# Kernel tuning notes

Measured on AMD Instinct MI355X. Metric: run time of the kernel, lower is better.

Reference implementation:

```python
import jax, jax.numpy as jnp
import numpy as np

N_EMBD = 384
N_HEAD = 6
HEAD_SIZE = N_EMBD // N_HEAD  # 64
B, T, S = 128, 256, 256
EPS = 1e-5


def setup_inputs() -> dict:
    key = jax.random.key(0)
    ks = jax.random.split(key, 20)
    w = lambda k, shape: (jax.random.normal(k, shape, dtype=jnp.float32) * 0.02)
    inp = {
        'x': jax.random.normal(ks[0], (B, T, N_EMBD), dtype=jnp.float32),
        'encoder_output': jax.random.normal(ks[1], (B, S, N_EMBD), dtype=jnp.float32),
        # masked self-attention heads (stacked over heads): [H, C, D]
        'wq1': w(ks[2], (N_HEAD, N_EMBD, HEAD_SIZE)),
        'wk1': w(ks[3], (N_HEAD, N_EMBD, HEAD_SIZE)),
        'wv1': w(ks[4], (N_HEAD, N_EMBD, HEAD_SIZE)),
        'proj1_w': w(ks[5], (N_EMBD, N_EMBD)),
        'proj1_b': jnp.zeros((N_EMBD,), jnp.float32),
        # cross-attention heads
        'wq2': w(ks[6], (N_HEAD, N_EMBD, HEAD_SIZE)),
        'wk2': w(ks[7], (N_HEAD, N_EMBD, HEAD_SIZE)),
        'wv2': w(ks[8], (N_HEAD, N_EMBD, HEAD_SIZE)),
        'proj2_w': w(ks[9], (N_EMBD, N_EMBD)),
        'proj2_b': jnp.zeros((N_EMBD,), jnp.float32),
        # feed-forward
        'ffn_w1': w(ks[10], (N_EMBD, 4 * N_EMBD)),
        'ffn_b1': jnp.zeros((4 * N_EMBD,), jnp.float32),
        'ffn_w2': w(ks[11], (4 * N_EMBD, N_EMBD)),
        'ffn_b2': jnp.zeros((N_EMBD,), jnp.float32),
        # layernorms
        'ln1_g': jnp.ones((N_EMBD,), jnp.float32), 'ln1_b': jnp.zeros((N_EMBD,), jnp.float32),
        'ln2_g': jnp.ones((N_EMBD,), jnp.float32), 'ln2_b': jnp.zeros((N_EMBD,), jnp.float32),
        'ln3_g': jnp.ones((N_EMBD,), jnp.float32), 'ln3_b': jnp.zeros((N_EMBD,), jnp.float32),
    }
    return inp


def _layernorm(x, g, b):
    mu = jnp.mean(x, axis=-1, keepdims=True)
    var = jnp.mean(jnp.square(x - mu), axis=-1, keepdims=True)
    return (x - mu) * jax.lax.rsqrt(var + EPS) * g + b


def _mha(xq, xkv, wq, wk, wv, proj_w, proj_b, causal):
    # NOTE: source scales by C**-0.5 with C = n_embd (not head_size)
    scale = jnp.asarray(N_EMBD, xq.dtype) ** -0.5
    q = jnp.einsum('btc,hcd->bhtd', xq, wq)
    k = jnp.einsum('bsc,hcd->bhsd', xkv, wk)
    v = jnp.einsum('bsc,hcd->bhsd', xkv, wv)
    wei = jnp.einsum('bhtd,bhsd->bhts', q, k) * scale
    if causal:
        Tq, Tk = xq.shape[1], xkv.shape[1]
        mask = jnp.tril(jnp.ones((Tq, Tk), dtype=bool))
        wei = jnp.where(mask, wei, jnp.asarray(-jnp.inf, wei.dtype))
    p = jax.nn.softmax(wei, axis=-1)  # dropout omitted (eval mode)
    o = jnp.einsum('bhts,bhsd->bhtd', p, v)
    Bq, H, Tq, D = o.shape
    o = o.transpose(0, 2, 1, 3).reshape(Bq, Tq, H * D)  # concat heads
    return o @ proj_w + proj_b


def reference(x, encoder_output,
              wq1, wk1, wv1, proj1_w, proj1_b,
              wq2, wk2, wv2, proj2_w, proj2_b,
              ffn_w1, ffn_b1, ffn_w2, ffn_b2,
              ln1_g, ln1_b, ln2_g, ln2_b, ln3_g, ln3_b):
    # x = x + masked self-attn(ln1(x))
    x = x + _mha(_layernorm(x, ln1_g, ln1_b), _layernorm(x, ln1_g, ln1_b),
                 wq1, wk1, wv1, proj1_w, proj1_b, causal=True)
    # x = x + cross-attn(ln2(x), encoder_output)  (no mask)
    x = x + _mha(_layernorm(x, ln2_g, ln2_b), encoder_output,
                 wq2, wk2, wv2, proj2_w, proj2_b, causal=False)
    # x = x + ffwd(ln3(x))
    h = _layernorm(x, ln3_g, ln3_b)
    x = x + (jax.nn.relu(h @ ffn_w1 + ffn_b1) @ ffn_w2 + ffn_b2)
    return x
```

## Files before the change

kernel.cpp:

```cpp
#include <hip/hip_runtime.h>
#include <hip/hip_bf16.h>

#define BB 128
#define TT 256
#define CC 384
#define HH 6
#define DD 64
#define NTOK 32768

typedef __attribute__((ext_vector_type(8))) short short8;
typedef __attribute__((ext_vector_type(4))) float f32x4;

__device__ __forceinline__ unsigned short f2bf(float f) {
  union { float f; unsigned int u; } v; v.f = f;
  unsigned int r = v.u + 0x7fff + ((v.u >> 16) & 1);
  return (unsigned short)(r >> 16);
}

__device__ __forceinline__ void glds16(const void* g, void* l) {
  __builtin_amdgcn_global_load_lds((const __attribute__((address_space(1))) void*)g,
                                   (__attribute__((address_space(3))) void*)l, 16, 0, 0);
}

__device__ __forceinline__ void vm_drain() {
  asm volatile("s_waitcnt vmcnt(0)" ::: "memory");
  __builtin_amdgcn_sched_barrier(0);
}

__global__ __launch_bounds__(256) void pack_t_k(
    const float* __restrict__ wq1, const float* __restrict__ wk1, const float* __restrict__ wv1,
    const float* __restrict__ wq2, const float* __restrict__ wk2, const float* __restrict__ wv2,
    const float* __restrict__ proj1_w, const float* __restrict__ proj2_w,
    const float* __restrict__ ffn_w1, const float* __restrict__ ffn_w2,
    unsigned short* __restrict__ W) {
  __shared__ unsigned short tile[64 * 72];
  const int id = blockIdx.x;
  const int tid = threadIdx.x;
  const float* src;
  unsigned short* dst;
  int ldIn, ldOut, i0, j0;
  if (id < 216) {
    int w = id / 36, rem = id - w * 36;
    int h = rem / 6, tr = rem - h * 6;
    const float* bases[6] = {wq1, wk1, wv1, wq2, wk2, wv2};
    const int dstOff[6] = {0, 147456, 294912, 442368, 589824, 737280};
    src = bases[w] + h * 24576;
    dst = W + dstOff[w] + h * 24576;
    ldIn = 64; ldOut = 384; i0 = tr * 64; j0 = 0;
  } else if (id < 288) {
    int t = id - 216;
    int which = t / 36; t -= which * 36;
    int tr = t / 6, tc = t - tr * 6;
    src = which ? proj2_w : proj1_w;
    dst = W + (which ? 1032192 : 884736);
    ldIn = 384; ldOut = 384; i0 = tr * 64; j0 = tc * 64;
  } else if (id < 432) {
    int t = id - 288;
    int tr = t / 24, tc = t - tr * 24;
    src = ffn_w1; dst = W + 1179648;
    ldIn = 1536; ldOut = 384; i0 = tr * 64; j0 = tc * 64;
  } else {
    int t = id - 432;
    int tr = t / 6, tc = t - tr * 6;
    src = ffn_w2; dst = W + 1769472;
    ldIn = 384; ldOut = 1536; i0 = tr * 64; j0 = tc * 64;
  }
#pragma unroll
  for (int p = 0; p < 4; ++p) {
    int chunk = p * 256 + tid;
    int r = chunk >> 4, c4 = chunk & 15;
    float4 f = *(const float4*)&src[(size_t)(i0 + r) * ldIn + j0 + c4 * 4];
    tile[(c4 * 4 + 0) * 72 + r] = f2bf(f.x);
    tile[(c4 * 4 + 1) * 72 + r] = f2bf(f.y);
    tile[(c4 * 4 + 2) * 72 + r] = f2bf(f.z);
    tile[(c4 * 4 + 3) * 72 + r] = f2bf(f.w);
  }
  __syncthreads();
#pragma unroll
  for (int p = 0; p < 2; ++p) {
    int chunk = p * 256 + tid;
    int j = chunk >> 3, i8 = chunk & 7;
    *(uint4*)&dst[(size_t)(j0 + j) * ldOut + i0 + i8 * 8] = *(const uint4*)&tile[j * 72 + i8 * 8];
  }
}

__global__ __launch_bounds__(256) void ln_k(const float* __restrict__ x,
                                            unsigned short* __restrict__ out,
                                            const float* __restrict__ gamma,
                                            const float* __restrict__ beta) {
  int row = blockIdx.x * 4 + (threadIdx.x >> 6);
  int lane = threadIdx.x & 63;
  const float* xr = x + (size_t)row * CC;
  float v[6];
  float s = 0.f;
#pragma unroll
  for (int j = 0; j < 6; ++j) { v[j] = xr[j * 64 + lane]; s += v[j]; }
#pragma unroll
  for (int m = 1; m < 64; m <<= 1) s += __shfl_xor(s, m);
  float mu = s * (1.0f / CC);
  float vs = 0.f;
#pragma unroll
  for (int j = 0; j < 6; ++j) { float d = v[j] - mu; vs += d * d; }
#pragma unroll
  for (int m = 1; m < 64; m <<= 1) vs += __shfl_xor(vs, m);
  float rs = rsqrtf(vs * (1.0f / CC) + 1e-5f);
  unsigned short* orow = out + (size_t)row * CC;
#pragma unroll
  for (int j = 0; j < 6; ++j) {
    int cidx = j * 64 + lane;
    orow[cidx] = f2bf((v[j] - mu) * rs * gamma[cidx] + beta[cidx]);
  }
}

template <int EPI, bool AF32, int BM>
__global__ __launch_bounds__(256) void gemm_k(const void* __restrict__ Ap, int lda,
                                              const unsigned short* __restrict__ Bt, int ldb,
                                              void* __restrict__ Cp, int ldc,
                                              const float* __restrict__ bias,
                                              const float* __restrict__ res, int ldres,
                                              int K, int nx) {
  constexpr int MI = BM / 32;
  constexpr int APASS = BM * 8 / 256;
  constexpr int SMEMN = (EPI == 2) ? (BM * 256) : (BM * 64 + 8192);
  __shared__ unsigned short smem[SMEMN];
  unsigned short* sA = smem;
  unsigned short* sB = smem + BM * 64;
  const int tid = threadIdx.x;
  const int chunkg = gridDim.x >> 3;
  const int wg = blockIdx.x;
  const int lg = (wg & 7) * chunkg + (wg >> 3);
  const int bx = lg % nx, by = lg / nx;
  const int m0 = by * BM;
  const int n0 = bx * 128;
  const int wid = tid >> 6, lane = tid & 63;
  const int wr = wid >> 1, wc = wid & 1;
  const int g = lane >> 4, c = lane & 15;

  f32x4 acc[MI][4] = {};
  float biasr[4];
  if (EPI >= 1) {
#pragma unroll
    for (int ni = 0; ni < 4; ++ni) biasr[ni] = bias[n0 + wc * 64 + ni * 16 + c];
  }

  const int nt = K >> 6;
  for (int t = 0; t < nt; ++t) {
    const int k0 = t * 64;
    if constexpr (!AF32) {
#pragma unroll
      for (int p = 0; p < APASS; ++p) {
        int chunk = p * 256 + tid;
        int row = chunk >> 3, grp = chunk & 7;
        const unsigned short* Ab = (const unsigned short*)Ap;
        glds16(&Ab[(size_t)(m0 + row) * lda + k0 + ((grp ^ (row & 7)) << 3)], &sA[chunk * 8]);
      }
    } else {
#pragma unroll
      for (int p = 0; p < APASS; ++p) {
        int chunk = p * 256 + tid;
        int row = chunk >> 3, grp = chunk & 7;
        int dst = row * 64 + ((grp ^ (row & 7)) << 3);
        const float* Af = (const float*)Ap + (size_t)(m0 + row) * lda + k0 + grp * 8;
        float4 f0 = *(const float4*)Af;
        float4 f1 = *(const float4*)(Af + 4);
        union { unsigned short h[8]; uint4 u; } t2;
        t2.h[0] = f2bf(f0.x); t2.h[1] = f2bf(f0.y); t2.h[2] = f2bf(f0.z); t2.h[3] = f2bf(f0.w);
        t2.h[4] = f2bf(f1.x); t2.h[5] = f2bf(f1.y); t2.h[6] = f2bf(f1.z); t2.h[7] = f2bf(f1.w);
        *(uint4*)&sA[dst] = t2.u;
      }
    }
#pragma unroll
    for (int p = 0; p < 4; ++p) {
      int chunk = p * 256 + tid;
      int row = chunk >> 3, grp = chunk & 7;
      glds16(&Bt[(size_t)(n0 + row) * ldb + k0 + ((grp ^ (row & 7)) << 3)], &sB[chunk * 8]);
    }
    vm_drain();
    __syncthreads();
#pragma unroll
    for (int kk = 0; kk < 2; ++kk) {
      short8 a[MI], b[4];
#pragma unroll
      for (int mi = 0; mi < MI; ++mi) {
        int r = wr * (BM / 2) + mi * 16 + c;
        a[mi] = *(const short8*)&sA[r * 64 + (((kk * 4 + g) ^ (r & 7)) << 3)];
      }
#pragma unroll
      for (int ni = 0; ni < 4; ++ni) {
        int rb = wc * 64 + ni * 16 + c;
        b[ni] = *(const short8*)&sB[rb * 64 + (((kk * 4 + g) ^ (rb & 7)) << 3)];
      }
#pragma unroll
      for (int mi = 0; mi < MI; ++mi)
#pragma unroll
        for (int ni = 0; ni < 4; ++ni)
          acc[mi][ni] = __builtin_amdgcn_mfma_f32_16x16x32_bf16(a[mi], b[ni], acc[mi][ni], 0, 0, 0);
    }
    __syncthreads();
  }

  if (EPI <= 1) {
#pragma unroll
    for (int mi = 0; mi < MI; ++mi)
#pragma unroll
      for (int ni = 0; ni < 4; ++ni)
#pragma unroll
        for (int i = 0; i < 4; ++i) {
          int row = wr * (BM / 2) + mi * 16 + g * 4 + i;
          int col = wc * 64 + ni * 16 + c;
          float v = acc[mi][ni][i];
          if (EPI == 1) v = fmaxf(v + biasr[ni], 0.f);
          int gsw = (col >> 3) ^ ((row >> 2) & 7);
          smem[row * 128 + gsw * 8 + (col & 7)] = f2bf(v);
        }
    __syncthreads();
#pragma unroll
    for (int it = 0; it < BM / 16; ++it) {
      int chunk = it * 256 + tid;
      int row = chunk >> 4, c16 = chunk & 15;
      int gsw = c16 ^ ((row >> 2) & 7);
      *(uint4*)&((unsigned short*)Cp)[(size_t)(m0 + row) * ldc + n0 + c16 * 8] =
          *(const uint4*)&smem[row * 128 + gsw * 8];
    }
  } else {
    float* smf = (float*)smem;
#pragma unroll
    for (int mi = 0; mi < MI; ++mi)
#pragma unroll
      for (int ni = 0; ni < 4; ++ni)
#pragma unroll
        for (int i = 0; i < 4; ++i) {
          int row = wr * (BM / 2) + mi * 16 + g * 4 + i;
          int col = wc * 64 + ni * 16 + c;
          int gg = col >> 2;
          int sg = gg ^ (row & 7);
          smf[row * 128 + sg * 4 + (col & 3)] = acc[mi][ni][i] + biasr[ni];
        }
    __syncthreads();
#pragma unroll
    for (int it = 0; it < BM / 8; ++it) {
      int chunk = it * 256 + tid;
      int row = chunk >> 5, gg = chunk & 31;
      int sg = gg ^ (row & 7);
      float4 v = *(const float4*)&smf[row * 128 + sg * 4];
      float4 r = *(const float4*)&res[(size_t)(m0 + row) * ldres + n0 + gg * 4];
      float4 o;
      o.x = v.x + r.x; o.y = v.y + r.y; o.z = v.z + r.z; o.w = v.w + r.w;
      *(float4*)&((float*)Cp)[(size_t)(m0 + row) * ldc + n0 + gg * 4] = o;
    }
  }
}

__device__ __forceinline__ int vt_off(int d, int sgrp) {
  return d * 256 + ((((sgrp + (d >> 3)) & 31) ^ (d & 7)) << 3);
}

template <bool CAUSAL>
__global__ __launch_bounds__(512, 2) void attn_k(const unsigned short* __restrict__ QKV,
                                                 unsigned short* __restrict__ O) {
  __shared__ unsigned short Ks[256 * 64];
  __shared__ unsigned short Vt[64 * 256];
  __shared__ unsigned short Ps[8][16 * 40];
  const int bh = blockIdx.x >> 1;
  const int half = blockIdx.x & 1;
  const int b = bh / HH, hh = bh - b * HH;
  const int tid = threadIdx.x, wid = tid >> 6, lane = tid & 63;
  const int g = lane >> 4, c = lane & 15;
  const unsigned short* base = QKV + (size_t)b * TT * 1152;

#pragma unroll
  for (int t = 0; t < 4; ++t) {
    int chunk = t * 512 + tid;
    int s = chunk >> 3, grp = chunk & 7;
    *(uint4*)&Ks[s * 64 + ((grp ^ (s & 7)) << 3)] =
        *(const uint4*)&base[(size_t)s * 1152 + 384 + hh * 64 + grp * 8];
    union { unsigned short h[8]; uint4 u; } tv;
    tv.u = *(const uint4*)&base[(size_t)s * 1152 + 768 + hh * 64 + grp * 8];
#pragma unroll
    for (int j = 0; j < 8; ++j) Vt[vt_off(grp * 8 + j, s >> 3) + (s & 7)] = tv.h[j];
  }
  __syncthreads();

  const float scale = 0.05103103630798287f;
  unsigned short* Pw = &Ps[wid][0];
  const int qr0 = half * 128 + wid * 16;

  short8 aq[2];
#pragma unroll
  for (int kk = 0; kk < 2; ++kk)
    aq[kk] = *(const short8*)&QKV[(size_t)(b * TT + qr0 + c) * 1152 + hh * 64 + kk * 32 + g * 8];

  f32x4 sacc[16] = {};
#pragma unroll
  for (int sj = 0; sj < 16; ++sj) {
    if (!CAUSAL || sj * 16 <= qr0) {
      int rk = sj * 16 + c;
      f32x4 z = sacc[sj];
      z = __builtin_amdgcn_mfma_f32_16x16x32_bf16(
          aq[0], *(const short8*)&Ks[rk * 64 + ((g ^ (rk & 7)) << 3)], z, 0, 0, 0);
      z = __builtin_amdgcn_mfma_f32_16x16x32_bf16(
          aq[1], *(const short8*)&Ks[rk * 64 + (((4 + g) ^ (rk & 7)) << 3)], z, 0, 0, 0);
      sacc[sj] = z;
    }
  }

  float inv[4];
#pragma unroll
  for (int i = 0; i < 4; ++i) {
    const int qr = qr0 + g * 4 + i;
    float mx = -1e30f;
#pragma unroll
    for (int sj = 0; sj < 16; ++sj) {
      if (!CAUSAL || sj * 16 <= qr0) {
        int s = sj * 16 + c;
        float v = sacc[sj][i] * scale;
        if (CAUSAL && s > qr) v = -1e30f;
        sacc[sj][i] = v;
        mx = fmaxf(mx, v);
      }
    }
#pragma unroll
    for (int m = 1; m < 16; m <<= 1) mx = fmaxf(mx, __shfl_xor(mx, m));
    float sum = 0.f;
#pragma unroll
    for (int sj = 0; sj < 16; ++sj) {
      if (!CAUSAL || sj * 16 <= qr0) {
        float p = __expf(sacc[sj][i] - mx);
        sacc[sj][i] = p;
        sum += p;
      }
    }
#pragma unroll
    for (int m = 1; m < 16; m <<= 1) sum += __shfl_xor(sum, m);
    inv[i] = 1.0f / sum;
  }

  f32x4 oacc[4] = {};
#pragma unroll
  for (int sk = 0; sk < 8; ++sk) {
    if (!CAUSAL || sk * 32 <= qr0) {
#pragma unroll
      for (int half_sj = 0; half_sj < 2; ++half_sj) {
        int sj = sk * 2 + half_sj;
#pragma unroll
        for (int i = 0; i < 4; ++i)
          Pw[(g * 4 + i) * 40 + half_sj * 16 + c] = f2bf(sacc[sj][i]);
      }
      short8 ap = *(const short8*)&Pw[c * 40 + g * 8];
#pragma unroll
      for (int dj = 0; dj < 4; ++dj) {
        short8 bv = *(const short8*)&Vt[vt_off(dj * 16 + c, sk * 4 + g)];
        oacc[dj] = __builtin_amdgcn_mfma_f32_16x16x32_bf16(ap, bv, oacc[dj], 0, 0, 0);
      }
    }
  }

  __syncthreads();
#pragma unroll
  for (int dj = 0; dj < 4; ++dj)
#pragma unroll
    for (int i = 0; i < 4; ++i) {
      int lr = wid * 16 + g * 4 + i;
      int col = dj * 16 + c;
      int gsw = (col >> 3) ^ ((lr >> 2) & 7);
      Ks[lr * 64 + gsw * 8 + (col & 7)] = f2bf(oacc[dj][i] * inv[i]);
    }
  __syncthreads();
#pragma unroll
  for (int it = 0; it < 2; ++it) {
    int chunk = it * 512 + tid;
    int row = chunk >> 3, c8 = chunk & 7;
    int gsw = c8 ^ ((row >> 2) & 7);
    *(uint4*)&O[(size_t)(b * TT + half * 128 + row) * CC + hh * 64 + c8 * 8] =
        *(const uint4*)&Ks[row * 64 + gsw * 8];
  }
}

extern "C" void kernel_launch(void* const* d_in, const int* in_sizes, int n_in,
                              void* d_out, int out_size, void* d_ws, size_t ws_size,
                              hipStream_t stream) {
  const float* x = (const float*)d_in[0];
  const float* enc = (const float*)d_in[1];
  const float* wq1 = (const float*)d_in[2];
  const float* wk1 = (const float*)d_in[3];
  const float* wv1 = (const float*)d_in[4];
  const float* proj1_w = (const float*)d_in[5];
  const float* proj1_b = (const float*)d_in[6];
  const float* wq2 = (const float*)d_in[7];
  const float* wk2 = (const float*)d_in[8];
  const float* wv2 = (const float*)d_in[9];
  const float* proj2_w = (const float*)d_in[10];
  const float* proj2_b = (const float*)d_in[11];
  const float* ffn_w1 = (const float*)d_in[12];
  const float* ffn_b1 = (const float*)d_in[13];
  const float* ffn_w2 = (const float*)d_in[14];
  const float* ffn_b2 = (const float*)d_in[15];
  const float* ln1_g = (const float*)d_in[16];
  const float* ln1_b = (const float*)d_in[17];
  const float* ln2_g = (const float*)d_in[18];
  const float* ln2_b = (const float*)d_in[19];
  const float* ln3_g = (const float*)d_in[20];
  const float* ln3_b = (const float*)d_in[21];
  float* out = (float*)d_out;

  char* ws = (char*)d_ws;
  const size_t OFF_A = 0;
  const size_t OFF_X = 50331648;
  const size_t OFF_Q = 75497472;
  const size_t OFF_O = 150994944;
  const size_t OFF_W = 176160768;

  float* xc = (float*)(ws + OFF_A);
  unsigned short* xn = (unsigned short*)(ws + OFF_X);
  unsigned short* qkv = (unsigned short*)(ws + OFF_Q);
  unsigned short* h1 = (unsigned short*)(ws + OFF_Q);
  unsigned short* obuf = (unsigned short*)(ws + OFF_O);
  unsigned short* W = (unsigned short*)(ws + OFF_W);

  unsigned short* Wqkv1t = W + 0;
  unsigned short* Wq2t = W + 442368;
  unsigned short* Wkv2t = W + 589824;
  unsigned short* proj1t = W + 884736;
  unsigned short* proj2t = W + 1032192;
  unsigned short* W1t = W + 1179648;
  unsigned short* W2t = W + 1769472;

  pack_t_k<<<576, 256, 0, stream>>>(wq1, wk1, wv1, wq2, wk2, wv2,
                                    proj1_w, proj2_w, ffn_w1, ffn_w2, W);

  dim3 blk(256);
  ln_k<<<8192, blk, 0, stream>>>(x, xn, ln1_g, ln1_b);
  gemm_k<0, false, 128><<<2304, blk, 0, stream>>>(xn, 384, Wqkv1t, 384, qkv, 1152,
                                                  nullptr, nullptr, 0, 384, 9);
  attn_k<true><<<1536, 512, 0, stream>>>(qkv, obuf);
  gemm_k<2, false, 64><<<1536, blk, 0, stream>>>(obuf, 384, proj1t, 384, xc, 384,
                                                 proj1_b, x, 384, 384, 3);
  ln_k<<<8192, blk, 0, stream>>>(xc, xn, ln2_g, ln2_b);
  gemm_k<0, false, 128><<<768, blk, 0, stream>>>(xn, 384, Wq2t, 384, qkv, 1152,
                                                 nullptr, nullptr, 0, 384, 3);
  gemm_k<0, true, 128><<<1536, blk, 0, stream>>>(enc, 384, Wkv2t, 384, qkv + 384, 1152,
                                                 nullptr, nullptr, 0, 384, 6);
  attn_k<false><<<1536, 512, 0, stream>>>(qkv, obuf);
  gemm_k<2, false, 64><<<1536, blk, 0, stream>>>(obuf, 384, proj2t, 384, xc, 384,
                                                 proj2_b, xc, 384, 384, 3);
  ln_k<<<8192, blk, 0, stream>>>(xc, xn, ln3_g, ln3_b);
  gemm_k<1, false, 128><<<3072, blk, 0, stream>>>(xn, 384, W1t, 384, h1, 1536,
                                                  ffn_b1, nullptr, 0, 384, 12);
  gemm_k<2, false, 64><<<1536, blk, 0, stream>>>(h1, 1536, W2t, 1536, out, 384,
                                                 ffn_b2, xc, 384, 1536, 3);
}
```

Measured before the change: 399.7 us.

## Double-buffer GEMM LDS tiles, shrink BM to 64, vectorize layernorm

The bf16-input GEMM path now double-buffers A/B tiles in LDS, issuing the next tile's global-to-LDS loads before computing the current one and waiting with a partial vmcnt. This hides global load latency that the old drain-then-compute loop exposed. Several GEMM launches switch from BM=128 to BM=64 with twice the blocks, trading per-block reuse for more parallelism and lower LDS/register use. The layernorm kernel also moves to float2 loads and packed 32-bit bf16 stores.

```diff
diff --git a/kernel.cpp b/kernel.cpp
--- a/kernel.cpp
+++ b/kernel.cpp
@@ -90,25 +90,32 @@
                                             const float* __restrict__ beta) {
   int row = blockIdx.x * 4 + (threadIdx.x >> 6);
   int lane = threadIdx.x & 63;
-  const float* xr = x + (size_t)row * CC;
-  float v[6];
+  const float2* xr = (const float2*)(x + (size_t)row * CC);
+  float2 v[3];
   float s = 0.f;
 #pragma unroll
-  for (int j = 0; j < 6; ++j) { v[j] = xr[j * 64 + lane]; s += v[j]; }
+  for (int j = 0; j < 3; ++j) { v[j] = xr[j * 64 + lane]; s += v[j].x + v[j].y; }
 #pragma unroll
   for (int m = 1; m < 64; m <<= 1) s += __shfl_xor(s, m);
   float mu = s * (1.0f / CC);
   float vs = 0.f;
 #pragma unroll
-  for (int j = 0; j < 6; ++j) { float d = v[j] - mu; vs += d * d; }
+  for (int j = 0; j < 3; ++j) {
+    float dx = v[j].x - mu, dy = v[j].y - mu;
+    vs += dx * dx + dy * dy;
+  }
 #pragma unroll
   for (int m = 1; m < 64; m <<= 1) vs += __shfl_xor(vs, m);
   float rs = rsqrtf(vs * (1.0f / CC) + 1e-5f);
-  unsigned short* orow = out + (size_t)row * CC;
-#pragma unroll
-  for (int j = 0; j < 6; ++j) {
+  unsigned int* orow = (unsigned int*)(out + (size_t)row * CC);
+#pragma unroll
+  for (int j = 0; j < 3; ++j) {
     int cidx = j * 64 + lane;
-    orow[cidx] = f2bf((v[j] - mu) * rs * gamma[cidx] + beta[cidx]);
+    float2 gmm = ((const float2*)gamma)[cidx];
+    float2 bt = ((const float2*)beta)[cidx];
+    unsigned int lo = f2bf((v[j].x - mu) * rs * gmm.x + bt.x);
+    unsigned int hi = f2bf((v[j].y - mu) * rs * gmm.y + bt.y);
+    orow[cidx] = lo | (hi << 16);
   }
 }
 
@@ -121,10 +128,9 @@
                                               int K, int nx) {
   constexpr int MI = BM / 32;
   constexpr int APASS = BM * 8 / 256;
-  constexpr int SMEMN = (EPI == 2) ? (BM * 256) : (BM * 64 + 8192);
+  constexpr int LOADS = APASS + 4;
+  constexpr int SMEMN = AF32 ? (BM * 64 + 8192) : 2 * (BM * 64 + 8192);
   __shared__ unsigned short smem[SMEMN];
-  unsigned short* sA = smem;
-  unsigned short* sB = smem + BM * 64;
   const int tid = threadIdx.x;
   const int chunkg = gridDim.x >> 3;
   const int wg = blockIdx.x;
@@ -142,19 +148,85 @@
 #pragma unroll
     for (int ni = 0; ni < 4; ++ni) biasr[ni] = bias[n0 + wc * 64 + ni * 16 + c];
   }
-
   const int nt = K >> 6;
-  for (int t = 0; t < nt; ++t) {
+
+  auto stageAB = [&](int t, unsigned short* sAb, unsigned short* sBb) {
     const int k0 = t * 64;
-    if constexpr (!AF32) {
-#pragma unroll
-      for (int p = 0; p < APASS; ++p) {
-        int chunk = p * 256 + tid;
-        int row = chunk >> 3, grp = chunk & 7;
-        const unsigned short* Ab = (const unsigned short*)Ap;
-        glds16(&Ab[(size_t)(m0 + row) * lda + k0 + ((grp ^ (row & 7)) << 3)], &sA[chunk * 8]);
-      }
-    } else {
+#pragma unroll
+    for (int p = 0; p < APASS; ++p) {
+      int chunk = p * 256 + tid;
+      int row = chunk >> 3, grp = chunk & 7;
+      const unsigned short* Ab = (const unsigned short*)Ap;
+      glds16(&Ab[(size_t)(m0 + row) * lda + k0 + ((grp ^ (row & 7)) << 3)], &sAb[chunk * 8]);
+    }
+#pragma unroll
+    for (int p = 0; p < 4; ++p) {
+      int chunk = p * 256 + tid;
+      int row = chunk >> 3, grp = chunk & 7;
+      glds16(&Bt[(size_t)(n0 + row) * ldb + k0 + ((grp ^ (row & 7)) << 3)], &sBb[chunk * 8]);
+    }
+  };
+  auto computeT = [&](const unsigned short* sAb, const unsigned short* sBb) {
+#pragma unroll
+    for (int kk = 0; kk < 2; ++kk) {
+      short8 a[MI], b[4];
+#pragma unroll
+      for (int mi = 0; mi < MI; ++mi) {
+        int r = wr * (BM / 2) + mi * 16 + c;
+        a[mi] = *(const short8*)&sAb[r * 64 + (((kk * 4 + g) ^ (r & 7)) << 3)];
+      }
+#pragma unroll
+      for (int ni = 0; ni < 4; ++ni) {
+        int rb = wc * 64 + ni * 16 + c;
+        b[ni] = *(const short8*)&sBb[rb * 64 + (((kk * 4 + g) ^ (rb & 7)) << 3)];
+      }
+#pragma unroll
+      for (int mi = 0; mi < MI; ++mi)
+#pragma unroll
+        for (int ni = 0; ni < 4; ++ni)
+          acc[mi][ni] = __builtin_amdgcn_mfma_f32_16x16x32_bf16(a[mi], b[ni], acc[mi][ni], 0, 0, 0);
+    }
+  };
+
+  if constexpr (!AF32) {
+    unsigned short* sA0 = smem;
+    unsigned short* sB0 = smem + BM * 64;
+    unsigned short* sA1 = smem + BM * 64 + 8192;
+    unsigned short* sB1 = sA1 + BM * 64;
+    stageAB(0, sA0, sB0);
+    int t = 0;
+    for (;;) {
+      if (t + 1 < nt) {
+        stageAB(t + 1, sA1, sB1);
+        asm volatile("s_waitcnt vmcnt(%0)" ::"i"(LOADS) : "memory");
+      } else {
+        asm volatile("s_waitcnt vmcnt(0)" ::: "memory");
+      }
+      __builtin_amdgcn_sched_barrier(0);
+      __builtin_amdgcn_s_barrier();
+      computeT(sA0, sB0);
+      if (t + 1 >= nt) break;
+      __builtin_amdgcn_s_barrier();
+      ++t;
+      if (t + 1 < nt) {
+        stageAB(t + 1, sA0, sB0);
+        asm volatile("s_waitcnt vmcnt(%0)" ::"i"(LOADS) : "memory");
+      } else {
+        asm volatile("s_waitcnt vmcnt(0)" ::: "memory");
+      }
+      __builtin_amdgcn_sched_barrier(0);
+      __builtin_amdgcn_s_barrier();
+      computeT(sA1, sB1);
+      if (t + 1 >= nt) break;
+      __builtin_amdgcn_s_barrier();
+      ++t;
+    }
+    __builtin_amdgcn_s_barrier();
+  } else {
+    unsigned short* sA = smem;
+    unsigned short* sB = smem + BM * 64;
+    for (int t = 0; t < nt; ++t) {
+      const int k0 = t * 64;
 #pragma unroll
       for (int p = 0; p < APASS; ++p) {
         int chunk = p * 256 + tid;
@@ -168,35 +240,17 @@
         t2.h[4] = f2bf(f1.x); t2.h[5] = f2bf(f1.y); t2.h[6] = f2bf(f1.z); t2.h[7] = f2bf(f1.w);
         *(uint4*)&sA[dst] = t2.u;
       }
-    }
-#pragma unroll
-    for (int p = 0; p < 4; ++p) {
-      int chunk = p * 256 + tid;
-      int row = chunk >> 3, grp = chunk & 7;
-      glds16(&Bt[(size_t)(n0 + row) * ldb + k0 + ((grp ^ (row & 7)) << 3)], &sB[chunk * 8]);
-    }
-    vm_drain();
-    __syncthreads();
-#pragma unroll
-    for (int kk = 0; kk < 2; ++kk) {
-      short8 a[MI], b[4];
-#pragma unroll
-      for (int mi = 0; mi < MI; ++mi) {
-        int r = wr * (BM / 2) + mi * 16 + c;
-        a[mi] = *(const short8*)&sA[r * 64 + (((kk * 4 + g) ^ (r & 7)) << 3)];
-      }
-#pragma unroll
-      for (int ni = 0; ni < 4; ++ni) {
-        int rb = wc * 64 + ni * 16 + c;
-        b[ni] = *(const short8*)&sB[rb * 64 + (((kk * 4 + g) ^ (rb & 7)) << 3)];
-      }
-#pragma unroll
-      for (int mi = 0; mi < MI; ++mi)
-#pragma unroll
-        for (int ni = 0; ni < 4; ++ni)
-          acc[mi][ni] = __builtin_amdgcn_mfma_f32_16x16x32_bf16(a[mi], b[ni], acc[mi][ni], 0, 0, 0);
-    }
-    __syncthreads();
+#pragma unroll
+      for (int p = 0; p < 4; ++p) {
+        int chunk = p * 256 + tid;
+        int row = chunk >> 3, grp = chunk & 7;
+        glds16(&Bt[(size_t)(n0 + row) * ldb + k0 + ((grp ^ (row & 7)) << 3)], &sB[chunk * 8]);
+      }
+      vm_drain();
+      __syncthreads();
+      computeT(sA, sB);
+      __syncthreads();
+    }
   }
 
   if (EPI <= 1) {
@@ -430,13 +484,13 @@
 
   dim3 blk(256);
   ln_k<<<8192, blk, 0, stream>>>(x, xn, ln1_g, ln1_b);
-  gemm_k<0, false, 128><<<2304, blk, 0, stream>>>(xn, 384, Wqkv1t, 384, qkv, 1152,
-                                                  nullptr, nullptr, 0, 384, 9);
+  gemm_k<0, false, 64><<<4608, blk, 0, stream>>>(xn, 384, Wqkv1t, 384, qkv, 1152,
+                                                 nullptr, nullptr, 0, 384, 9);
   attn_k<true><<<1536, 512, 0, stream>>>(qkv, obuf);
   gemm_k<2, false, 64><<<1536, blk, 0, stream>>>(obuf, 384, proj1t, 384, xc, 384,
                                                  proj1_b, x, 384, 384, 3);
   ln_k<<<8192, blk, 0, stream>>>(xc, xn, ln2_g, ln2_b);
-  gemm_k<0, false, 128><<<768, blk, 0, stream>>>(xn, 384, Wq2t, 384, qkv, 1152,
+  gemm_k<0, false, 64><<<1536, blk, 0, stream>>>(xn, 384, Wq2t, 384, qkv, 1152,
                                                  nullptr, nullptr, 0, 384, 3);
   gemm_k<0, true, 128><<<1536, blk, 0, stream>>>(enc, 384, Wkv2t, 384, qkv + 384, 1152,
                                                  nullptr, nullptr, 0, 384, 6);
@@ -444,8 +498,8 @@
   gemm_k<2, false, 64><<<1536, blk, 0, stream>>>(obuf, 384, proj2t, 384, xc, 384,
                                                  proj2_b, xc, 384, 384, 3);
   ln_k<<<8192, blk, 0, stream>>>(xc, xn, ln3_g, ln3_b);
-  gemm_k<1, false, 128><<<3072, blk, 0, stream>>>(xn, 384, W1t, 384, h1, 1536,
-                                                  ffn_b1, nullptr, 0, 384, 12);
+  gemm_k<1, false, 64><<<6144, blk, 0, stream>>>(xn, 384, W1t, 384, h1, 1536,
+                                                 ffn_b1, nullptr, 0, 384, 12);
   gemm_k<2, false, 64><<<1536, blk, 0, stream>>>(h1, 1536, W2t, 1536, out, 384,
                                                  ffn_b2, xc, 384, 1536, 3);
 }
```

After: 410.8 us. +2.8%, slower.

## Fuse projection GEMM with residual add and following LayerNorm

Applied to the files above, without the earlier changes.

Adds a gemm_ln_k kernel in which each block computes a full 64x384 output row tile of the attention projection, adds bias and residual, writes the fp32 residual stream, and computes the next LayerNorm in the epilogue using a cross-wave partial sum reduction before writing bf16 normalized output. This removes two separate LayerNorm launches and their reread of the residual stream. The fused kernel runs only 512 blocks with a single-buffered K loop, so occupancy and latency hiding may be worse than the old GEMM. The variance is computed as E[x^2]-mu^2, which is less numerically robust. The remaining ln_k is also vectorized to float2 loads and packed bf16 stores.

```diff
diff --git a/kernel.cpp b/kernel.cpp
--- a/kernel.cpp
+++ b/kernel.cpp
@@ -90,25 +90,32 @@
                                             const float* __restrict__ beta) {
   int row = blockIdx.x * 4 + (threadIdx.x >> 6);
   int lane = threadIdx.x & 63;
-  const float* xr = x + (size_t)row * CC;
-  float v[6];
+  const float2* xr = (const float2*)(x + (size_t)row * CC);
+  float2 v[3];
   float s = 0.f;
 #pragma unroll
-  for (int j = 0; j < 6; ++j) { v[j] = xr[j * 64 + lane]; s += v[j]; }
+  for (int j = 0; j < 3; ++j) { v[j] = xr[j * 64 + lane]; s += v[j].x + v[j].y; }
 #pragma unroll
   for (int m = 1; m < 64; m <<= 1) s += __shfl_xor(s, m);
   float mu = s * (1.0f / CC);
   float vs = 0.f;
 #pragma unroll
-  for (int j = 0; j < 6; ++j) { float d = v[j] - mu; vs += d * d; }
+  for (int j = 0; j < 3; ++j) {
+    float dx = v[j].x - mu, dy = v[j].y - mu;
+    vs += dx * dx + dy * dy;
+  }
 #pragma unroll
   for (int m = 1; m < 64; m <<= 1) vs += __shfl_xor(vs, m);
   float rs = rsqrtf(vs * (1.0f / CC) + 1e-5f);
-  unsigned short* orow = out + (size_t)row * CC;
-#pragma unroll
-  for (int j = 0; j < 6; ++j) {
+  unsigned int* orow = (unsigned int*)(out + (size_t)row * CC);
+#pragma unroll
+  for (int j = 0; j < 3; ++j) {
     int cidx = j * 64 + lane;
-    orow[cidx] = f2bf((v[j] - mu) * rs * gamma[cidx] + beta[cidx]);
+    float2 gmm = ((const float2*)gamma)[cidx];
+    float2 bt = ((const float2*)beta)[cidx];
+    unsigned int lo = f2bf((v[j].x - mu) * rs * gmm.x + bt.x);
+    unsigned int hi = f2bf((v[j].y - mu) * rs * gmm.y + bt.y);
+    orow[cidx] = lo | (hi << 16);
   }
 }
 
@@ -248,6 +255,153 @@
       o.x = v.x + r.x; o.y = v.y + r.y; o.z = v.z + r.z; o.w = v.w + r.w;
       *(float4*)&((float*)Cp)[(size_t)(m0 + row) * ldc + n0 + gg * 4] = o;
     }
+  }
+}
+
+__global__ __launch_bounds__(512, 2) void gemm_ln_k(
+    const unsigned short* __restrict__ Ab, const unsigned short* __restrict__ Bt,
+    const float* __restrict__ bias, const float* __restrict__ res,
+    float* __restrict__ xc, const float* __restrict__ gamma,
+    const float* __restrict__ beta, unsigned short* __restrict__ xn) {
+  __shared__ unsigned short smem[28672];
+  __shared__ float part[64][8];
+  unsigned short* sA = smem;
+  unsigned short* sB = smem + 4096;
+  const int tid = threadIdx.x;
+  const int chunkg = gridDim.x >> 3;
+  const int wg = blockIdx.x;
+  const int lg = (wg & 7) * chunkg + (wg >> 3);
+  const int m0 = lg * 64;
+  const int wid = tid >> 6, lane = tid & 63;
+  const int wr = wid >> 2, wcg = wid & 3;
+  const int g = lane >> 4, c = lane & 15;
+
+  f32x4 acc[2][6] = {};
+  float biasr[6], gam[6], bet[6];
+#pragma unroll
+  for (int ni = 0; ni < 6; ++ni) {
+    int col = wcg * 96 + ni * 16 + c;
+    biasr[ni] = bias[col]; gam[ni] = gamma[col]; bet[ni] = beta[col];
+  }
+
+  for (int t = 0; t < 6; ++t) {
+    const int k0 = t * 64;
+    {
+      int chunk = tid;
+      int row = chunk >> 3, grp = chunk & 7;
+      glds16(&Ab[(size_t)(m0 + row) * 384 + k0 + ((grp ^ (row & 7)) << 3)], &sA[chunk * 8]);
+    }
+#pragma unroll
+    for (int p = 0; p < 6; ++p) {
+      int chunk = p * 512 + tid;
+      int row = chunk >> 3, grp = chunk & 7;
+      glds16(&Bt[(size_t)row * 384 + k0 + ((grp ^ (row & 7)) << 3)], &sB[chunk * 8]);
+    }
+    vm_drain();
+    __syncthreads();
+#pragma unroll
+    for (int kk = 0; kk < 2; ++kk) {
+      short8 a[2], b[6];
+#pragma unroll
+      for (int mi = 0; mi < 2; ++mi) {
+        int r = wr * 32 + mi * 16 + c;
+        a[mi] = *(const short8*)&sA[r * 64 + (((kk * 4 + g) ^ (r & 7)) << 3)];
+      }
+#pragma unroll
+      for (int ni = 0; ni < 6; ++ni) {
+        int rb = wcg * 96 + ni * 16 + c;
+        b[ni] = *(const short8*)&sB[rb * 64 + (((kk * 4 + g) ^ (rb & 7)) << 3)];
+      }
+#pragma unroll
+      for (int mi = 0; mi < 2; ++mi)
+#pragma unroll
+        for (int ni = 0; ni < 6; ++ni)
+          acc[mi][ni] = __builtin_amdgcn_mfma_f32_16x16x32_bf16(a[mi], b[ni], acc[mi][ni], 0, 0, 0);
+    }
+    __syncthreads();
+  }
+
+#pragma unroll
+  for (int mi = 0; mi < 2; ++mi)
+#pragma unroll
+    for (int i = 0; i < 4; ++i) {
+      int row = m0 + wr * 32 + mi * 16 + g * 4 + i;
+#pragma unroll
+      for (int ni = 0; ni < 6; ++ni)
+        acc[mi][ni][i] += biasr[ni] + res[(size_t)row * 384 + wcg * 96 + ni * 16 + c];
+    }
+
+#pragma unroll
+  for (int mi = 0; mi < 2; ++mi)
+#pragma unroll
+    for (int i = 0; i < 4; ++i) {
+      float s = 0.f, q = 0.f;
+#pragma unroll
+      for (int ni = 0; ni < 6; ++ni) { float v = acc[mi][ni][i]; s += v; q += v * v; }
+#pragma unroll
+      for (int m = 1; m < 16; m <<= 1) { s += __shfl_xor(s, m); q += __shfl_xor(q, m); }
+      if (c == 0) {
+        int lr = wr * 32 + mi * 16 + g * 4 + i;
+        part[lr][wcg] = s;
+        part[lr][4 + wcg] = q;
+      }
+    }
+  __syncthreads();
+  float mu[2][4], rs[2][4];
+#pragma unroll
+  for (int mi = 0; mi < 2; ++mi)
+#pragma unroll
+    for (int i = 0; i < 4; ++i) {
+      int lr = wr * 32 + mi * 16 + g * 4 + i;
+      float s = part[lr][0] + part[lr][1] + part[lr][2] + part[lr][3];
+      float q = part[lr][4] + part[lr][5] + part[lr][6] + part[lr][7];
+      float m_ = s * (1.0f / 384.f);
+      mu[mi][i] = m_;
+      rs[mi][i] = rsqrtf(q * (1.0f / 384.f) - m_ * m_ + 1e-5f);
+    }
+
+  float* bf = (float*)smem;
+#pragma unroll
+  for (int h = 0; h < 2; ++h) {
+    __syncthreads();
+    if (wr == h) {
+#pragma unroll
+      for (int mi = 0; mi < 2; ++mi)
+#pragma unroll
+        for (int ni = 0; ni < 6; ++ni)
+#pragma unroll
+          for (int i = 0; i < 4; ++i) {
+            int lr = mi * 16 + g * 4 + i;
+            bf[lr * 388 + wcg * 96 + ni * 16 + c] = acc[mi][ni][i];
+          }
+    }
+    __syncthreads();
+#pragma unroll
+    for (int p = 0; p < 6; ++p) {
+      int chunk = p * 512 + tid;
+      int row = chunk / 96, gg = chunk % 96;
+      float4 v = *(const float4*)&bf[row * 388 + gg * 4];
+      *(float4*)&xc[(size_t)(m0 + h * 32 + row) * 384 + gg * 4] = v;
+    }
+  }
+
+  __syncthreads();
+#pragma unroll
+  for (int mi = 0; mi < 2; ++mi)
+#pragma unroll
+    for (int ni = 0; ni < 6; ++ni)
+#pragma unroll
+      for (int i = 0; i < 4; ++i) {
+        int lr = wr * 32 + mi * 16 + g * 4 + i;
+        smem[lr * 392 + wcg * 96 + ni * 16 + c] =
+            f2bf((acc[mi][ni][i] - mu[mi][i]) * rs[mi][i] * gam[ni] + bet[ni]);
+      }
+  __syncthreads();
+#pragma unroll
+  for (int p = 0; p < 6; ++p) {
+    int chunk = p * 512 + tid;
+    int row = chunk / 48, c8 = chunk % 48;
+    *(uint4*)&xn[(size_t)(m0 + row) * 384 + c8 * 8] = *(const uint4*)&smem[row * 392 + c8 * 8];
   }
 }
 
@@ -433,17 +587,13 @@
   gemm_k<0, false, 128><<<2304, blk, 0, stream>>>(xn, 384, Wqkv1t, 384, qkv, 1152,
                                                   nullptr, nullptr, 0, 384, 9);
   attn_k<true><<<1536, 512, 0, stream>>>(qkv, obuf);
-  gemm_k<2, false, 64><<<1536, blk, 0, stream>>>(obuf, 384, proj1t, 384, xc, 384,
-                                                 proj1_b, x, 384, 384, 3);
-  ln_k<<<8192, blk, 0, stream>>>(xc, xn, ln2_g, ln2_b);
+  gemm_ln_k<<<512, 512, 0, stream>>>(obuf, proj1t, proj1_b, x, xc, ln2_g, ln2_b, xn);
   gemm_k<0, false, 128><<<768, blk, 0, stream>>>(xn, 384, Wq2t, 384, qkv, 1152,
                                                  nullptr, nullptr, 0, 384, 3);
   gemm_k<0, true, 128><<<1536, blk, 0, stream>>>(enc, 384, Wkv2t, 384, qkv + 384, 1152,
                                                  nullptr, nullptr, 0, 384, 6);
   attn_k<false><<<1536, 512, 0, stream>>>(qkv, obuf);
-  gemm_k<2, false, 64><<<1536, blk, 0, stream>>>(obuf, 384, proj2t, 384, xc, 384,
-                                                 proj2_b, xc, 384, 384, 3);
-  ln_k<<<8192, blk, 0, stream>>>(xc, xn, ln3_g, ln3_b);
+  gemm_ln_k<<<512, 512, 0, stream>>>(obuf, proj2t, proj2_b, xc, xc, ln3_g, ln3_b, xn);
   gemm_k<1, false, 128><<<3072, blk, 0, stream>>>(xn, 384, W1t, 384, h1, 1536,
                                                   ffn_b1, nullptr, 0, 384, 12);
   gemm_k<2, false, 64><<<1536, blk, 0, stream>>>(h1, 1536, W2t, 1536, out, 384,
```

Measured after the change: 399.2 us. No clear change (-0.1%).
